# Kernel optimization log

Measured on AMD Instinct MI355X. Metric: run time of the kernel, lower is better.

Reference implementation:

```python
import jax, jax.numpy as jnp
import numpy as np

IN_CH, OUT_CH, KS = 64, 128, 3
GRID, DEG = 8, 3
STRIDE, PAD = 1, 1
SIZE = IN_CH * KS * KS            # 576
NCOEF = GRID + DEG                # 11
GRID_RANGE = (-1.0, 1.0)


def _xavier_uniform(key, shape):
    fan_out, fan_in = shape
    a = float(np.sqrt(6.0 / (fan_in + fan_out)))
    return jax.random.uniform(key, shape, minval=-a, maxval=a, dtype=jnp.float32)


def setup_inputs() -> dict:
    key = jax.random.key(0)
    k1, k2, k3 = jax.random.split(key, 3)
    x = jax.random.normal(k1, (8, IN_CH, 32, 32), dtype=jnp.float32)
    # non-trainable knot grid, one row per unfolded feature
    knots = jnp.tile(jnp.linspace(GRID_RANGE[0], GRID_RANGE[1], GRID + 1, dtype=jnp.float32)[None, :], (SIZE, 1))
    coeff = 0.1 * jax.random.normal(k2, (OUT_CH, SIZE, NCOEF), dtype=jnp.float32)
    base_weights = _xavier_uniform(k3, (OUT_CH, SIZE))
    spline_weights = jnp.ones((OUT_CH, SIZE), dtype=jnp.float32)
    return {"x": x, "knots": knots, "coeff": coeff,
            "base_weights": base_weights, "spline_weights": spline_weights}


def bspline_basis(x, grid, k):
    # x: (S, P) evaluation points; grid: (S, G+1) knots. Returns (S, G+k, P).
    h = (grid[:, -1:] - grid[:, :1]) / (grid.shape[1] - 1)
    left = grid[:, :1] - h * jnp.arange(k, 0, -1, dtype=x.dtype)
    right = grid[:, -1:] + h * jnp.arange(1, k + 1, dtype=x.dtype)
    g = jnp.concatenate([left, grid, right], axis=1)  # (S, G+1+2k)
    xe = x[:, None, :]
    B = ((xe >= g[:, :-1, None]) & (xe < g[:, 1:, None])).astype(x.dtype)
    for d in range(1, k + 1):  # de Boor recursion over fixed degree
        B = ((xe - g[:, :-(d + 1), None]) / (g[:, d:-1, None] - g[:, :-(d + 1), None]) * B[:, :-1]
             + (g[:, d + 1:, None] - xe) / (g[:, d + 1:, None] - g[:, 1:-d, None]) * B[:, 1:])
    return B


def _unfold(x):
    # torch F.unfold with channel-major (c, kh, kw) feature ordering
    N, C, H, W = x.shape
    xp = jnp.pad(x, ((0, 0), (0, 0), (PAD, PAD), (PAD, PAD)))
    Hp = (H + 2 * PAD - KS) // STRIDE + 1
    Wp = (W + 2 * PAD - KS) // STRIDE + 1
    patches = jnp.stack([xp[:, :, i:i + STRIDE * Hp:STRIDE, j:j + STRIDE * Wp:STRIDE]
                         for i in range(KS) for j in range(KS)], axis=2)  # (N, C, KS*KS, Hp, Wp)
    L = Hp * Wp
    u = patches.reshape(N, SIZE, L)              # (N, size, L)
    u = jnp.transpose(u, (1, 0, 2)).reshape(SIZE, N * L)  # (size, N*L), col = n*L + l
    return u, Hp, Wp


def reference(x, knots, coeff, base_weights, spline_weights):
    N = x.shape[0]
    u, Hp, Wp = _unfold(x)                                   # (size, P)
    base = base_weights @ jax.nn.silu(u)                     # (Cout, P)
    B = bspline_basis(u, knots, DEG)                         # (size, ncoef, P)
    eff = spline_weights[:, :, None] * coeff                 # (Cout, size, ncoef)
    spl = jnp.einsum('csj,sjp->cp', eff, B)                  # (Cout, P)
    out = (base + spl).reshape(OUT_CH, N, Hp, Wp)
    return jnp.transpose(out, (1, 0, 2, 3))                  # (N, Cout, Hp, Wp)
```

## Files before the change

### kernel.cpp

```cpp
#include <hip/hip_runtime.h>


typedef __attribute__((ext_vector_type(8))) short bf16x8;
typedef __attribute__((ext_vector_type(4))) float f32x4;
typedef __attribute__((ext_vector_type(16))) float f32x16;
typedef __attribute__((ext_vector_type(4))) unsigned short u16x4;

#define WSWZ_BYTES 1769472
#define PHI_OFF    WSWZ_BYTES
#define PHI_BYTES  14205696
#define PART_OFF   (PHI_OFF + PHI_BYTES)

__device__ __forceinline__ short f2bf(float f) {
    union { float f; unsigned u; } c; c.f = f;
    unsigned r = c.u + 0x7fffu + ((c.u >> 16) & 1u);
    return (short)(r >> 16);
}
__device__ __forceinline__ float bf2f(unsigned short u) {
    union { unsigned u; float f; } c; c.u = ((unsigned)u) << 16;
    return c.f;
}

__global__ void kan_prep(const float* __restrict__ coeff,
                         const float* __restrict__ basew,
                         const float* __restrict__ splw,
                         const float* __restrict__ x,
                         short* __restrict__ Wswz,
                         short* __restrict__ Phi) {
    __shared__ float coeffL[6336];
    __shared__ float basewL[576];
    __shared__ float splwL[576];
    __shared__ unsigned short xs[64 * 32];
    const int t = threadIdx.x;

    if (blockIdx.x < 272) {
        const int rowid = blockIdx.x;
        const int n     = rowid / 34;
        const int ypad  = rowid - n * 34;
        const int y     = ypad - 1;
        const bool yvalid = (y >= 0 && y < 32);

        if (yvalid) {
#pragma unroll
            for (int it = 0; it < 2; ++it) {
                int cg = t + it * 256;
                int ci = cg >> 3, q = cg & 7;
                f32x4 v = *(const f32x4*)(x + (((n * 64 + ci) * 32 + y) * 32 + q * 4));
                u16x4 p;
                p.x = (unsigned short)f2bf(v.x); p.y = (unsigned short)f2bf(v.y);
                p.z = (unsigned short)f2bf(v.z); p.w = (unsigned short)f2bf(v.w);
                *(u16x4*)&xs[ci * 32 + q * 4] = p;
            }
        }
        __syncthreads();

        const size_t rowbase = (size_t)rowid * 12 * 2176;
        for (int it = t; it < 272; it += 256) {
            int xp = it >> 3, cch = it & 7, c0 = cch << 3;
            bool interior = yvalid && (xp >= 1 && xp <= 32);
            int px = xp - 1;
            int pxc = px < 0 ? 0 : (px > 31 ? 31 : px);
            bf16x8 packs[12];
#pragma unroll
            for (int j = 0; j < 8; ++j) {
                float v = interior ? bf2f(xs[(c0 + j) * 32 + pxc]) : 0.f;
                float tt = 4.f * v + 7.f;
                int   i0 = -100;
                float b0 = 0.f, b1 = 0.f, b2 = 0.f, b3 = 0.f;
                if (tt >= 0.f && tt < 14.f) {
                    i0 = (int)tt;
                    float fr  = tt - (float)i0;
                    float omf = 1.f - fr;
                    float fr2 = fr * fr, fr3 = fr2 * fr;
                    b0 = omf * omf * omf * (1.f / 6.f);
                    b1 = (3.f * fr3 - 6.f * fr2 + 4.f) * (1.f / 6.f);
                    b2 = (-3.f * fr3 + 3.f * fr2 + 3.f * fr + 1.f) * (1.f / 6.f);
                    b3 = fr3 * (1.f / 6.f);
                }
                float silu = v * __builtin_amdgcn_rcpf(1.f + __expf(-v));
                packs[0][j] = f2bf(silu);
#pragma unroll
                for (int f = 1; f < 12; ++f) {
                    int jj = f - 1;
                    float val = 0.f;
                    val = (jj == i0 - 3) ? b0 : val;
                    val = (jj == i0 - 2) ? b1 : val;
                    val = (jj == i0 - 1) ? b2 : val;
                    val = (jj == i0    ) ? b3 : val;
                    packs[f][j] = f2bf(val);
                }
            }
            int swz = (cch ^ (xp & 7)) << 3;
#pragma unroll
            for (int f = 0; f < 12; ++f)
                *(bf16x8*)&Phi[rowbase + (size_t)f * 2176 + xp * 64 + swz] = packs[f];
        }
    } else {
        const int co = blockIdx.x - 272;
        const float* crow = coeff + co * 6336;
        for (int i = t; i < 6336; i += 256) coeffL[i] = crow[i];
        for (int i = t; i < 576; i += 256) {
            basewL[i] = basew[co * 576 + i];
            splwL[i]  = splw[co * 576 + i];
        }
        __syncthreads();
        const int cb = co >> 5, lm = co & 31;
        for (int c = t; c < 864; c += 256) {
            int kk16 = c >> 1, kh = c & 1;
            int f  = kk16 / 36;
            int rm = kk16 - f * 36;
            int tap = rm >> 2, q = rm & 3;
            bf16x8 pack;
#pragma unroll
            for (int j = 0; j < 8; ++j) {
                int ci = q * 16 + kh * 8 + j;
                int s  = ci * 9 + tap;
                float v = (f == 0) ? basewL[s] : splwL[s] * coeffL[s * 11 + (f - 1)];
                pack[j] = f2bf(v);
            }
            *(bf16x8*)(Wswz + (size_t)((kk16 * 4 + cb) * 64 + kh * 32 + lm) * 8) = pack;
        }
    }
}

__global__ __launch_bounds__(512, 2)
void kan_gemm(const short* __restrict__ Phi,
              const short* __restrict__ Wswz,
              float* __restrict__ part) {
    __shared__ short Bs[2 * 8704];

    const int t  = threadIdx.x;
    const int w8 = t >> 6;
    const int cb = w8 & 3;
    const int p  = w8 >> 2;
    const int l  = t & 63;
    const int ln = l & 31;
    const int kh = l >> 5;

    const int fg    = blockIdx.x >> 7;
    const int ptile = blockIdx.x & 127;
    const int n     = ptile >> 4;
    const int y0    = (ptile & 15) << 1;

    const char* phiB = (const char*)Phi;
    const int planeBase = (n * 34 + y0) * 12 + fg * 2;
#pragma unroll
    for (int k = 0; k < 5; ++k) {
        int i = t + k * 512;
        if (i < 2176) {
            int pl  = i / 1088;
            int r2  = i - pl * 1088;
            int row = r2 / 272;
            int m   = r2 - row * 272;
            const char* s = phiB + (size_t)(planeBase + row * 12 + pl) * 4352 + m * 16;
            __builtin_amdgcn_global_load_lds(
                (const __attribute__((address_space(1))) unsigned int*)s,
                (__attribute__((address_space(3))) unsigned int*)((char*)Bs + i * 16),
                16, 0, 0);
        }
    }

    const int kbase = (fg * 2 + p) * 36;
    const short* Abase = Wswz + (size_t)cb * 512 + (size_t)l * 8;
    bf16x8 ag[36];
#pragma unroll
    for (int g = 0; g < 36; ++g) {
        int q  = g / 9;
        int r9 = g - q * 9;
        int dx = r9 / 3;
        int dy = r9 - dx * 3;
        ag[g] = *(const bf16x8*)(Abase + (size_t)(kbase + (dy * 3 + dx) * 4 + q) * 2048);
    }

    __syncthreads();

    f32x16 acc[2];
#pragma unroll
    for (int pb = 0; pb < 2; ++pb)
#pragma unroll
        for (int r = 0; r < 16; ++r)
            acc[pb][r] = 0.f;

    const short* B0 = Bs + p * 8704;
#pragma unroll
    for (int q = 0; q < 4; ++q) {
#pragma unroll
        for (int dx = 0; dx < 3; ++dx) {
            const int g0 = (q * 3 + dx) * 3;
            const int c   = q * 2 + kh;
            const int key = (ln + dx) & 7;
            const int colb = (ln + dx) * 64 + ((c ^ key) << 3);
            bf16x8 b0 = *(const bf16x8*)&B0[0 * 2176 + colb];
            bf16x8 b1 = *(const bf16x8*)&B0[1 * 2176 + colb];
            bf16x8 b2 = *(const bf16x8*)&B0[2 * 2176 + colb];
            bf16x8 b3 = *(const bf16x8*)&B0[3 * 2176 + colb];
            acc[0] = __builtin_amdgcn_mfma_f32_32x32x16_bf16(ag[g0 + 0], b0, acc[0], 0, 0, 0);
            acc[1] = __builtin_amdgcn_mfma_f32_32x32x16_bf16(ag[g0 + 0], b1, acc[1], 0, 0, 0);
            acc[0] = __builtin_amdgcn_mfma_f32_32x32x16_bf16(ag[g0 + 1], b1, acc[0], 0, 0, 0);
            acc[1] = __builtin_amdgcn_mfma_f32_32x32x16_bf16(ag[g0 + 1], b2, acc[1], 0, 0, 0);
            acc[0] = __builtin_amdgcn_mfma_f32_32x32x16_bf16(ag[g0 + 2], b2, acc[0], 0, 0, 0);
            acc[1] = __builtin_amdgcn_mfma_f32_32x32x16_bf16(ag[g0 + 2], b3, acc[1], 0, 0, 0);
        }
    }

    __syncthreads();
    float* ex = (float*)Bs;
    if (p == 1) {
#pragma unroll
        for (int pb = 0; pb < 2; ++pb)
#pragma unroll
            for (int r = 0; r < 16; ++r) {
                int v = pb * 16 + r;
                ex[cb * 2048 + l * 32 + ((v + l) & 31)] = acc[pb][r];
            }
    }
    __syncthreads();
    if (p == 0) {
#pragma unroll
        for (int pb = 0; pb < 2; ++pb)
#pragma unroll
            for (int r = 0; r < 16; ++r) {
                int v = pb * 16 + r;
                acc[pb][r] += ex[cb * 2048 + l * 32 + ((v + l) & 31)];
            }

        float* dst = part + (size_t)fg * 1048576;
#pragma unroll
        for (int pb = 0; pb < 2; ++pb) {
            int y = y0 + pb;
#pragma unroll
            for (int r = 0; r < 16; ++r) {
                int row = (r & 3) + 8 * (r >> 2) + 4 * kh;
                int co  = cb * 32 + row;
                dst[((size_t)(n * 128 + co) * 32 + y) * 32 + ln] = acc[pb][r];
            }
        }
    }
}

__global__ void kan_reduce(const float* __restrict__ part,
                           float* __restrict__ out) {
    const int r = blockIdx.x;
    const int p = r & 127;
    const int i = r >> 7;
    const int n  = p >> 4;
    const int yp = p & 15;
    const int c  = i * 256 + threadIdx.x;
    const int co = c >> 4;
    const int rem = c & 15;
    const int yy = rem >> 3, xq = rem & 7;
    const size_t idx = ((size_t)(n * 128 + co) * 32 + yp * 2 + yy) * 8 + xq;
    f32x4 a = ((const f32x4*)part)[idx];
#pragma unroll
    for (int s = 1; s < 6; ++s)
        a += ((const f32x4*)(part + (size_t)s * 1048576))[idx];
    ((f32x4*)out)[idx] = a;
}

extern "C" void kernel_launch(void* const* d_in, const int* in_sizes, int n_in,
                              void* d_out, int out_size, void* d_ws, size_t ws_size,
                              hipStream_t stream) {
    const float* x     = (const float*)d_in[0];
    const float* coeff = (const float*)d_in[2];
    const float* basew = (const float*)d_in[3];
    const float* splw  = (const float*)d_in[4];
    float* out = (float*)d_out;

    short* Wswz = (short*)d_ws;
    short* Phi  = (short*)((char*)d_ws + PHI_OFF);
    float* part = (float*)((char*)d_ws + PART_OFF);

    kan_prep<<<400, 256, 0, stream>>>(coeff, basew, splw, x, Wswz, Phi);
    kan_gemm<<<768, 512, 0, stream>>>(Phi, Wswz, part);
    kan_reduce<<<1024, 256, 0, stream>>>(part, out);
}
```

Before: 110.4 us.

## Replace split-K partial sums and reduce kernel with in-block K reduction

The GEMM kernel is restructured so each block covers the full K range. Its eight waves are split into four K-quarters, each looping over three feature planes, with the next plane's LDS staging double-buffered behind the MFMA work. Partial sums are combined through LDS and written straight to the output. This removes the partial buffer write/read and the separate reduce launch, at the cost of fewer blocks (256 instead of 768), one block per CU, larger LDS use, and A fragments now loaded from global memory inside the loop instead of preloaded into registers.

```diff
diff --git a/kernel.cpp b/kernel.cpp
--- a/kernel.cpp
+++ b/kernel.cpp
@@ -9,7 +9,6 @@
 #define WSWZ_BYTES 1769472
 #define PHI_OFF    WSWZ_BYTES
 #define PHI_BYTES  14205696
-#define PART_OFF   (PHI_OFF + PHI_BYTES)
 
 __device__ __forceinline__ short f2bf(float f) {
     union { float f; unsigned u; } c; c.f = f;
@@ -123,55 +122,47 @@
     }
 }
 
-__global__ __launch_bounds__(512, 2)
-void kan_gemm(const short* __restrict__ Phi,
-              const short* __restrict__ Wswz,
-              float* __restrict__ part) {
-    __shared__ short Bs[2 * 8704];
+__global__ __launch_bounds__(512, 1)
+void kan_gemm2(const short* __restrict__ Phi,
+               const short* __restrict__ Wswz,
+               float* __restrict__ out) {
+    __shared__ __align__(16) char Bbuf[2 * 69632];
 
     const int t  = threadIdx.x;
     const int w8 = t >> 6;
-    const int cb = w8 & 3;
-    const int p  = w8 >> 2;
+    const int cb = w8 & 1;
+    const int fq = w8 >> 1;
     const int l  = t & 63;
     const int ln = l & 31;
     const int kh = l >> 5;
 
-    const int fg    = blockIdx.x >> 7;
+    const int ch    = blockIdx.x >> 7;
     const int ptile = blockIdx.x & 127;
     const int n     = ptile >> 4;
     const int y0    = (ptile & 15) << 1;
+    const int cbg   = ch * 2 + cb;
 
     const char* phiB = (const char*)Phi;
-    const int planeBase = (n * 34 + y0) * 12 + fg * 2;
-#pragma unroll
-    for (int k = 0; k < 5; ++k) {
-        int i = t + k * 512;
-        if (i < 2176) {
-            int pl  = i / 1088;
-            int r2  = i - pl * 1088;
-            int row = r2 / 272;
-            int m   = r2 - row * 272;
-            const char* s = phiB + (size_t)(planeBase + row * 12 + pl) * 4352 + m * 16;
-            __builtin_amdgcn_global_load_lds(
-                (const __attribute__((address_space(1))) unsigned int*)s,
-                (__attribute__((address_space(3))) unsigned int*)((char*)Bs + i * 16),
-                16, 0, 0);
-        }
-    }
-
-    const int kbase = (fg * 2 + p) * 36;
-    const short* Abase = Wswz + (size_t)cb * 512 + (size_t)l * 8;
-    bf16x8 ag[36];
-#pragma unroll
-    for (int g = 0; g < 36; ++g) {
-        int q  = g / 9;
-        int r9 = g - q * 9;
-        int dx = r9 / 3;
-        int dy = r9 - dx * 3;
-        ag[g] = *(const bf16x8*)(Abase + (size_t)(kbase + (dy * 3 + dx) * 4 + q) * 2048);
-    }
-
+    const int rowPlane = (n * 34 + y0) * 12;
+    auto stage = [&](int r, int buf) {
+#pragma unroll
+        for (int k = 0; k < 9; ++k) {
+            int i = t + k * 512;
+            if (i < 4352) {
+                int sfq = i / 1088;
+                int rem = i - sfq * 1088;
+                int row = rem / 272;
+                int m   = rem - row * 272;
+                const char* s = phiB + (size_t)(rowPlane + row * 12 + sfq * 3 + r) * 4352 + m * 16;
+                __builtin_amdgcn_global_load_lds(
+                    (const __attribute__((address_space(1))) unsigned int*)s,
+                    (__attribute__((address_space(3))) unsigned int*)(Bbuf + buf * 69632 + i * 16),
+                    16, 0, 0);
+            }
+        }
+    };
+
+    stage(0, 0);
     __syncthreads();
 
     f32x16 acc[2];
@@ -181,80 +172,74 @@
         for (int r = 0; r < 16; ++r)
             acc[pb][r] = 0.f;
 
-    const short* B0 = Bs + p * 8704;
-#pragma unroll
-    for (int q = 0; q < 4; ++q) {
-#pragma unroll
-        for (int dx = 0; dx < 3; ++dx) {
-            const int g0 = (q * 3 + dx) * 3;
-            const int c   = q * 2 + kh;
-            const int key = (ln + dx) & 7;
-            const int colb = (ln + dx) * 64 + ((c ^ key) << 3);
-            bf16x8 b0 = *(const bf16x8*)&B0[0 * 2176 + colb];
-            bf16x8 b1 = *(const bf16x8*)&B0[1 * 2176 + colb];
-            bf16x8 b2 = *(const bf16x8*)&B0[2 * 2176 + colb];
-            bf16x8 b3 = *(const bf16x8*)&B0[3 * 2176 + colb];
-            acc[0] = __builtin_amdgcn_mfma_f32_32x32x16_bf16(ag[g0 + 0], b0, acc[0], 0, 0, 0);
-            acc[1] = __builtin_amdgcn_mfma_f32_32x32x16_bf16(ag[g0 + 0], b1, acc[1], 0, 0, 0);
-            acc[0] = __builtin_amdgcn_mfma_f32_32x32x16_bf16(ag[g0 + 1], b1, acc[0], 0, 0, 0);
-            acc[1] = __builtin_amdgcn_mfma_f32_32x32x16_bf16(ag[g0 + 1], b2, acc[1], 0, 0, 0);
-            acc[0] = __builtin_amdgcn_mfma_f32_32x32x16_bf16(ag[g0 + 2], b2, acc[0], 0, 0, 0);
-            acc[1] = __builtin_amdgcn_mfma_f32_32x32x16_bf16(ag[g0 + 2], b3, acc[1], 0, 0, 0);
-        }
-    }
-
-    __syncthreads();
-    float* ex = (float*)Bs;
-    if (p == 1) {
+    const short* Abase = Wswz + (size_t)cbg * 512 + (size_t)l * 8;
+
+#pragma unroll 1
+    for (int r = 0; r < 3; ++r) {
+        const int buf = r & 1;
+        if (r < 2) stage(r + 1, buf ^ 1);
+
+        const short* B0 = (const short*)(Bbuf + buf * 69632 + fq * 17408);
+        const int kbase = (fq * 3 + r) * 36;
+#pragma unroll
+        for (int q = 0; q < 4; ++q) {
+#pragma unroll
+            for (int dx = 0; dx < 3; ++dx) {
+                bf16x8 a0 = *(const bf16x8*)(Abase + (size_t)(kbase + (0 * 3 + dx) * 4 + q) * 2048);
+                bf16x8 a1 = *(const bf16x8*)(Abase + (size_t)(kbase + (1 * 3 + dx) * 4 + q) * 2048);
+                bf16x8 a2 = *(const bf16x8*)(Abase + (size_t)(kbase + (2 * 3 + dx) * 4 + q) * 2048);
+                const int c   = q * 2 + kh;
+                const int key = (ln + dx) & 7;
+                const int colb = (ln + dx) * 64 + ((c ^ key) << 3);
+                bf16x8 b0 = *(const bf16x8*)&B0[0 * 2176 + colb];
+                bf16x8 b1 = *(const bf16x8*)&B0[1 * 2176 + colb];
+                bf16x8 b2 = *(const bf16x8*)&B0[2 * 2176 + colb];
+                bf16x8 b3 = *(const bf16x8*)&B0[3 * 2176 + colb];
+                acc[0] = __builtin_amdgcn_mfma_f32_32x32x16_bf16(a0, b0, acc[0], 0, 0, 0);
+                acc[1] = __builtin_amdgcn_mfma_f32_32x32x16_bf16(a0, b1, acc[1], 0, 0, 0);
+                acc[0] = __builtin_amdgcn_mfma_f32_32x32x16_bf16(a1, b1, acc[0], 0, 0, 0);
+                acc[1] = __builtin_amdgcn_mfma_f32_32x32x16_bf16(a1, b2, acc[1], 0, 0, 0);
+                acc[0] = __builtin_amdgcn_mfma_f32_32x32x16_bf16(a2, b2, acc[0], 0, 0, 0);
+                acc[1] = __builtin_amdgcn_mfma_f32_32x32x16_bf16(a2, b3, acc[1], 0, 0, 0);
+            }
+        }
+        __syncthreads();
+    }
+
+    float* ex = (float*)Bbuf;
+    if (fq != 0) {
+        const int slot = (fq - 1) * 2 + cb;
 #pragma unroll
         for (int pb = 0; pb < 2; ++pb)
 #pragma unroll
             for (int r = 0; r < 16; ++r) {
                 int v = pb * 16 + r;
-                ex[cb * 2048 + l * 32 + ((v + l) & 31)] = acc[pb][r];
+                ex[slot * 2048 + l * 32 + ((v + l) & 31)] = acc[pb][r];
             }
     }
     __syncthreads();
-    if (p == 0) {
-#pragma unroll
-        for (int pb = 0; pb < 2; ++pb)
-#pragma unroll
-            for (int r = 0; r < 16; ++r) {
-                int v = pb * 16 + r;
-                acc[pb][r] += ex[cb * 2048 + l * 32 + ((v + l) & 31)];
-            }
-
-        float* dst = part + (size_t)fg * 1048576;
+    if (fq == 0) {
+#pragma unroll
+        for (int s = 0; s < 3; ++s)
+#pragma unroll
+            for (int pb = 0; pb < 2; ++pb)
+#pragma unroll
+                for (int r = 0; r < 16; ++r) {
+                    int v = pb * 16 + r;
+                    acc[pb][r] += ex[(s * 2 + cb) * 2048 + l * 32 + ((v + l) & 31)];
+                }
+
 #pragma unroll
         for (int pb = 0; pb < 2; ++pb) {
             int y = y0 + pb;
 #pragma unroll
             for (int r = 0; r < 16; ++r) {
                 int row = (r & 3) + 8 * (r >> 2) + 4 * kh;
-                int co  = cb * 32 + row;
-                dst[((size_t)(n * 128 + co) * 32 + y) * 32 + ln] = acc[pb][r];
-            }
-        }
-    }
-}
-
-__global__ void kan_reduce(const float* __restrict__ part,
-                           float* __restrict__ out) {
-    const int r = blockIdx.x;
-    const int p = r & 127;
-    const int i = r >> 7;
-    const int n  = p >> 4;
-    const int yp = p & 15;
-    const int c  = i * 256 + threadIdx.x;
-    const int co = c >> 4;
-    const int rem = c & 15;
-    const int yy = rem >> 3, xq = rem & 7;
-    const size_t idx = ((size_t)(n * 128 + co) * 32 + yp * 2 + yy) * 8 + xq;
-    f32x4 a = ((const f32x4*)part)[idx];
-#pragma unroll
-    for (int s = 1; s < 6; ++s)
-        a += ((const f32x4*)(part + (size_t)s * 1048576))[idx];
-    ((f32x4*)out)[idx] = a;
+                int co  = cbg * 32 + row;
+                out[((size_t)(n * 128 + co) * 32 + y) * 32 + ln] = acc[pb][r];
+            }
+        }
+    }
 }
 
 extern "C" void kernel_launch(void* const* d_in, const int* in_sizes, int n_in,
@@ -268,9 +253,7 @@
 
     short* Wswz = (short*)d_ws;
     short* Phi  = (short*)((char*)d_ws + PHI_OFF);
-    float* part = (float*)((char*)d_ws + PART_OFF);
 
     kan_prep<<<400, 256, 0, stream>>>(coeff, basew, splw, x, Wswz, Phi);
-    kan_gemm<<<768, 512, 0, stream>>>(Phi, Wswz, part);
-    kan_reduce<<<1024, 256, 0, stream>>>(part, out);
-}
+    kan_gemm2<<<256, 512, 0, stream>>>(Phi, Wswz, out);
+}
```

New measurement: 102.7 us. -6.9%, faster.
